# Performance work log

Measured on AMD Instinct MI355X. Metric: run time of the kernel, lower is better.

Reference implementation:

```python
import jax, jax.numpy as jnp
import numpy as np

D_MODEL = 1024
NUM_EXPERTS = 64
TOP_K = 2
TEMPERATURE = 1.0


def setup_inputs() -> dict:
    key = jax.random.key(0)
    k1, k2, k3, k4 = jax.random.split(key, 4)
    mh_output = jax.random.normal(k1, (8, 4096, D_MODEL), dtype=jnp.float32)
    noise = jax.random.normal(k2, (8, 4096, NUM_EXPERTS), dtype=jnp.float32)  # randn_like sample, externalized
    # nn.Linear weights: shape [out, in], init normal(0, 0.02); biases zero
    W_route = jax.random.normal(k3, (NUM_EXPERTS, D_MODEL), dtype=jnp.float32) * 0.02
    b_route = jnp.zeros((NUM_EXPERTS,), dtype=jnp.float32)
    W_noise = jax.random.normal(k4, (NUM_EXPERTS, D_MODEL), dtype=jnp.float32) * 0.02
    b_noise = jnp.zeros((NUM_EXPERTS,), dtype=jnp.float32)
    return {"mh_output": mh_output, "noise": noise, "W_route": W_route,
            "b_route": b_route, "W_noise": W_noise, "b_noise": b_noise}


def reference(mh_output, noise, W_route, b_route, W_noise, b_noise):
    # logits = topkroute_linear(mh_output); noise_logits = noise_linear(mh_output)
    logits = jnp.einsum('bsd,ed->bse', mh_output, W_route) + b_route
    noise_logits = jnp.einsum('bsd,ed->bse', mh_output, W_noise) + b_noise
    # noisy logits = logits + temperature * randn * softplus(noise_logits)
    noisy = logits + TEMPERATURE * noise * jax.nn.softplus(noise_logits)
    # top-k, scatter into -inf, softmax  ==  softmax over top-k values scattered into zeros
    top_vals, indices = jax.lax.top_k(noisy, TOP_K)          # [b, s, k]
    probs_k = jax.nn.softmax(top_vals, axis=-1)              # softmax(-inf elsewhere) -> 0 elsewhere
    one_hot = jax.nn.one_hot(indices, NUM_EXPERTS, dtype=noisy.dtype)  # [b, s, k, E]
    router_output = jnp.sum(one_hot * probs_k[..., None], axis=-2)     # [b, s, E]
    return router_output, indices
```

## Files before the change

### kernel.cpp

```cpp
#include <hip/hip_runtime.h>
#include <math.h>


#define T_TOKENS 32768
#define D_MODEL  1024
#define NE       64
#define NCOL     128
#define M_TILE   32
#define NCHUNK   (D_MODEL / 32)
#define CS_LD    68
#define OUT_IDX_BASE ((size_t)T_TOKENS * NE)
#define W_ELEMS  (NCOL * D_MODEL)

typedef short  bf16x8  __attribute__((ext_vector_type(8)));
typedef float  floatx4 __attribute__((ext_vector_type(4)));

__device__ __forceinline__ unsigned short f32_to_bf16_rne(float x) {
    unsigned u = __float_as_uint(x);
    unsigned r = u + 0x7fffu + ((u >> 16) & 1u);
    return (unsigned short)(r >> 16);
}
__device__ __forceinline__ float bf16_bits_to_f32(unsigned short h) {
    return __uint_as_float(((unsigned)h) << 16);
}
__device__ __forceinline__ int4 pack8(const unsigned short* h) {
    int4 r;
    r.x = (int)((unsigned)h[0] | ((unsigned)h[1] << 16));
    r.y = (int)((unsigned)h[2] | ((unsigned)h[3] << 16));
    r.z = (int)((unsigned)h[4] | ((unsigned)h[5] << 16));
    r.w = (int)((unsigned)h[6] | ((unsigned)h[7] << 16));
    return r;
}
__device__ __forceinline__ float softplus_f(float x) {
    return fmaxf(x, 0.f) + log1pf(expf(-fabsf(x)));
}

__global__ __launch_bounds__(256) void prepack_w(
    const float* __restrict__ Wr, const float* __restrict__ Wn,
    short* __restrict__ Bh, short* __restrict__ Bl)
{
    int g   = blockIdx.x * 256 + threadIdx.x;
    int n   = g & 15;
    int kg  = (g >> 4) & 127;
    int t2  = g >> 11;
    int col = t2 * 16 + n;
    const float* src = (col < NE ? Wr + (size_t)col * D_MODEL
                                 : Wn + (size_t)(col - NE) * D_MODEL) + kg * 8;
    float4 a = *(const float4*)src;
    float4 b = *(const float4*)(src + 4);
    float v[8] = {a.x, a.y, a.z, a.w, b.x, b.y, b.z, b.w};
    unsigned short h[8], l[8];
    #pragma unroll
    for (int j = 0; j < 8; ++j) {
        h[j] = f32_to_bf16_rne(v[j]);
        l[j] = f32_to_bf16_rne(v[j] - bf16_bits_to_f32(h[j]));
    }
    *(int4*)(Bh + (size_t)g * 8) = pack8(h);
    *(int4*)(Bl + (size_t)g * 8) = pack8(l);
}

__global__ __launch_bounds__(256, 4) void router_mfma(
    const float* __restrict__ A,
    const float* __restrict__ noise,
    const float* __restrict__ br,
    const float* __restrict__ bn,
    const short* __restrict__ Bh,
    const short* __restrict__ Bl,
    float* __restrict__ out)
{
    __shared__ float Cs[M_TILE * CS_LD];
    __shared__ float s_p1[M_TILE], s_p2[M_TILE];
    __shared__ int   s_e1[M_TILE], s_e2[M_TILE];

    const int tid  = threadIdx.x;
    const int lane = tid & 63;
    const int wid  = tid >> 6;
    const int wm   = wid & 1;
    const int wn   = wid >> 1;
    const int n16  = lane & 15;
    const int quad = lane >> 4;
    const int m0   = blockIdx.x * M_TILE;

    const float* pA = A + (size_t)(m0 + wm * 16 + n16) * D_MODEL + quad * 8;

    int bBase[4];
    #pragma unroll
    for (int f = 0; f < 4; ++f) {
        int ntile = (f < 2) ? (wn * 2 + f) : (4 + wn * 2 + (f - 2));
        bBase[f] = ((ntile * 128 + quad) * 16 + n16) * 8;
    }

    floatx4 acc[4];
    #pragma unroll
    for (int f = 0; f < 4; ++f) acc[f] = (floatx4)0.f;

    float4 aC0 = *(const float4*)(pA);
    float4 aC1 = *(const float4*)(pA + 4);
    float4 aN0 = *(const float4*)(pA + 32);
    float4 aN1 = *(const float4*)(pA + 36);

    for (int kc = 0; kc < NCHUNK; ++kc) {
        float4 aF0, aF1;
        if (kc + 2 < NCHUNK) {
            aF0 = *(const float4*)(pA + (kc + 2) * 32);
            aF1 = *(const float4*)(pA + (kc + 2) * 32 + 4);
        }
        bf16x8 bh[4], bl[4];
        #pragma unroll
        for (int f = 0; f < 4; ++f) {
            size_t o = (size_t)bBase[f] + (size_t)kc * 512;
            bh[f] = *(const bf16x8*)(Bh + o);
            bl[f] = *(const bf16x8*)(Bl + o);
        }
        float v[8] = {aC0.x, aC0.y, aC0.z, aC0.w, aC1.x, aC1.y, aC1.z, aC1.w};
        bf16x8 afh, afl;
        #pragma unroll
        for (int j = 0; j < 8; ++j) {
            unsigned short h = f32_to_bf16_rne(v[j]);
            afh[j] = (short)h;
            afl[j] = (short)f32_to_bf16_rne(v[j] - bf16_bits_to_f32(h));
        }
        #pragma unroll
        for (int f = 0; f < 4; ++f) {
            acc[f] = __builtin_amdgcn_mfma_f32_16x16x32_bf16(afh, bh[f], acc[f], 0, 0, 0);
            acc[f] = __builtin_amdgcn_mfma_f32_16x16x32_bf16(afh, bl[f], acc[f], 0, 0, 0);
            acc[f] = __builtin_amdgcn_mfma_f32_16x16x32_bf16(afl, bh[f], acc[f], 0, 0, 0);
        }
        aC0 = aN0; aC1 = aN1; aN0 = aF0; aN1 = aF1;
    }

    #pragma unroll
    for (int nfi = 0; nfi < 2; ++nfi) {
        int e = wn * 32 + nfi * 16 + n16;
        float brv = br[e], bnv = bn[e];
        #pragma unroll
        for (int r = 0; r < 4; ++r) {
            int t = wm * 16 + quad * 4 + r;
            float nz    = noise[(size_t)(m0 + t) * NE + e];
            float route = acc[nfi][r]     + brv;
            float nl    = acc[2 + nfi][r] + bnv;
            Cs[t * CS_LD + e] = fmaf(nz, softplus_f(nl), route);
        }
    }
    __syncthreads();

    if (tid < M_TILE) {
        const int t = tid;
        float v1 = -INFINITY, v2 = -INFINITY;
        int e1 = 0, e2 = 0;
        #pragma unroll 8
        for (int e = 0; e < NE; ++e) {
            float v = Cs[t * CS_LD + e];
            if (v > v1) { v2 = v1; e2 = e1; v1 = v; e1 = e; }
            else if (v > v2) { v2 = v; e2 = e; }
        }
        float ex = expf(v2 - v1);
        float denom = 1.f + ex;
        s_p1[t] = 1.f / denom;
        s_p2[t] = ex / denom;
        s_e1[t] = e1;
        s_e2[t] = e2;
        float2 iv = make_float2((float)e1, (float)e2);
        *(float2*)(out + OUT_IDX_BASE + (size_t)(m0 + t) * 2) = iv;
    }
    __syncthreads();

    #pragma unroll
    for (int i = 0; i < 2; ++i) {
        int gi = i * 256 + tid;
        int t  = gi >> 4;
        int e0 = (gi & 15) * 4;
        float p1 = s_p1[t], p2 = s_p2[t];
        int   e1 = s_e1[t], e2 = s_e2[t];
        float4 v;
        v.x = (e0 + 0 == e1) ? p1 : ((e0 + 0 == e2) ? p2 : 0.f);
        v.y = (e0 + 1 == e1) ? p1 : ((e0 + 1 == e2) ? p2 : 0.f);
        v.z = (e0 + 2 == e1) ? p1 : ((e0 + 2 == e2) ? p2 : 0.f);
        v.w = (e0 + 3 == e1) ? p1 : ((e0 + 3 == e2) ? p2 : 0.f);
        *(float4*)(out + (size_t)(m0 + t) * NE + e0) = v;
    }
}

extern "C" void kernel_launch(void* const* d_in, const int* in_sizes, int n_in,
                              void* d_out, int out_size, void* d_ws, size_t ws_size,
                              hipStream_t stream) {
    const float* A     = (const float*)d_in[0];
    const float* noise = (const float*)d_in[1];
    const float* Wr    = (const float*)d_in[2];
    const float* br    = (const float*)d_in[3];
    const float* Wn    = (const float*)d_in[4];
    const float* bn    = (const float*)d_in[5];
    float* out = (float*)d_out;

    short* Bh = (short*)d_ws;
    short* Bl = Bh + W_ELEMS;

    prepack_w<<<dim3(W_ELEMS / 8 / 256), dim3(256), 0, stream>>>(Wr, Wn, Bh, Bl);
    router_mfma<<<dim3(T_TOKENS / M_TILE), dim3(256), 0, stream>>>(A, noise, br, bn, Bh, Bl, out);
}
```

Baseline: 268.9 us.

## Stage A tile as split bf16 in double-buffered LDS shared by all waves

Each thread now loads one float4 of the activation tile, converts it to hi/lo bf16 once, and writes it to a double-buffered shared-memory tile. Waves read the A fragments from there. Previously every wave converted its own A fragments, so the same conversion was repeated across waves. The wave split changes from 2x2 (M x N) to 4 waves over N, so each wave covers both 16-row M fragments with a single route/noise column tile, and the B fragments are prefetched one chunk ahead. The cost is a block barrier every K chunk and extra LDS traffic.

New measurement: 232.6 us. 1.16x faster.

```diff
diff --git a/kernel.cpp b/kernel.cpp
--- a/kernel.cpp
+++ b/kernel.cpp
@@ -22,14 +22,6 @@
 }
 __device__ __forceinline__ float bf16_bits_to_f32(unsigned short h) {
     return __uint_as_float(((unsigned)h) << 16);
-}
-__device__ __forceinline__ int4 pack8(const unsigned short* h) {
-    int4 r;
-    r.x = (int)((unsigned)h[0] | ((unsigned)h[1] << 16));
-    r.y = (int)((unsigned)h[2] | ((unsigned)h[3] << 16));
-    r.z = (int)((unsigned)h[4] | ((unsigned)h[5] << 16));
-    r.w = (int)((unsigned)h[6] | ((unsigned)h[7] << 16));
-    return r;
 }
 __device__ __forceinline__ float softplus_f(float x) {
     return fmaxf(x, 0.f) + log1pf(expf(-fabsf(x)));
@@ -55,8 +47,17 @@
         h[j] = f32_to_bf16_rne(v[j]);
         l[j] = f32_to_bf16_rne(v[j] - bf16_bits_to_f32(h[j]));
     }
-    *(int4*)(Bh + (size_t)g * 8) = pack8(h);
-    *(int4*)(Bl + (size_t)g * 8) = pack8(l);
+    int4 hp, lp;
+    hp.x = (int)((unsigned)h[0] | ((unsigned)h[1] << 16));
+    hp.y = (int)((unsigned)h[2] | ((unsigned)h[3] << 16));
+    hp.z = (int)((unsigned)h[4] | ((unsigned)h[5] << 16));
+    hp.w = (int)((unsigned)h[6] | ((unsigned)h[7] << 16));
+    lp.x = (int)((unsigned)l[0] | ((unsigned)l[1] << 16));
+    lp.y = (int)((unsigned)l[2] | ((unsigned)l[3] << 16));
+    lp.z = (int)((unsigned)l[4] | ((unsigned)l[5] << 16));
+    lp.w = (int)((unsigned)l[6] | ((unsigned)l[7] << 16));
+    *(int4*)(Bh + (size_t)g * 8) = hp;
+    *(int4*)(Bl + (size_t)g * 8) = lp;
 }
 
 __global__ __launch_bounds__(256, 4) void router_mfma(
@@ -68,6 +69,8 @@
     const short* __restrict__ Bl,
     float* __restrict__ out)
 {
+    __shared__ __align__(16) short Ah[2][M_TILE * 32];
+    __shared__ __align__(16) short Al[2][M_TILE * 32];
     __shared__ float Cs[M_TILE * CS_LD];
     __shared__ float s_p1[M_TILE], s_p2[M_TILE];
     __shared__ int   s_e1[M_TILE], s_e2[M_TILE];
@@ -75,72 +78,107 @@
     const int tid  = threadIdx.x;
     const int lane = tid & 63;
     const int wid  = tid >> 6;
-    const int wm   = wid & 1;
-    const int wn   = wid >> 1;
     const int n16  = lane & 15;
     const int quad = lane >> 4;
     const int m0   = blockIdx.x * M_TILE;
 
-    const float* pA = A + (size_t)(m0 + wm * 16 + n16) * D_MODEL + quad * 8;
-
-    int bBase[4];
+    const int ms = tid >> 3;
+    const int kq = tid & 7;
+    const float* pA = A + (size_t)(m0 + ms) * D_MODEL + kq * 4;
+    const int sBase = ((kq >> 1) * M_TILE + ms) * 8 + (kq & 1) * 4;
+
+    const int bBaseR = ((wid * 128 + quad) * 16 + n16) * 8;
+    const int bBaseN = (((4 + wid) * 128 + quad) * 16 + n16) * 8;
+
+    floatx4 acc[2][2];
     #pragma unroll
-    for (int f = 0; f < 4; ++f) {
-        int ntile = (f < 2) ? (wn * 2 + f) : (4 + wn * 2 + (f - 2));
-        bBase[f] = ((ntile * 128 + quad) * 16 + n16) * 8;
-    }
-
-    floatx4 acc[4];
-    #pragma unroll
-    for (int f = 0; f < 4; ++f) acc[f] = (floatx4)0.f;
-
-    float4 aC0 = *(const float4*)(pA);
-    float4 aC1 = *(const float4*)(pA + 4);
-    float4 aN0 = *(const float4*)(pA + 32);
-    float4 aN1 = *(const float4*)(pA + 36);
+    for (int i = 0; i < 2; ++i) { acc[i][0] = (floatx4)0.f; acc[i][1] = (floatx4)0.f; }
+
+#define CONVERT_STORE(buf_, f4_) do {                                       \
+        float v_[4] = {(f4_).x, (f4_).y, (f4_).z, (f4_).w};                  \
+        unsigned short h_[4], l_[4];                                         \
+        _Pragma("unroll")                                                    \
+        for (int j_ = 0; j_ < 4; ++j_) {                                     \
+            h_[j_] = f32_to_bf16_rne(v_[j_]);                                \
+            l_[j_] = f32_to_bf16_rne(v_[j_] - bf16_bits_to_f32(h_[j_]));     \
+        }                                                                    \
+        int2 hp_, lp_;                                                       \
+        hp_.x = (int)((unsigned)h_[0] | ((unsigned)h_[1] << 16));            \
+        hp_.y = (int)((unsigned)h_[2] | ((unsigned)h_[3] << 16));            \
+        lp_.x = (int)((unsigned)l_[0] | ((unsigned)l_[1] << 16));            \
+        lp_.y = (int)((unsigned)l_[2] | ((unsigned)l_[3] << 16));            \
+        *(int2*)&Ah[(buf_)][sBase] = hp_;                                    \
+        *(int2*)&Al[(buf_)][sBase] = lp_;                                    \
+    } while (0)
+
+    {
+        float4 a0 = *(const float4*)pA;
+        CONVERT_STORE(0, a0);
+    }
+    bf16x8 bhR, blR, bhN, blN;
+    bhR = *(const bf16x8*)(Bh + bBaseR);
+    blR = *(const bf16x8*)(Bl + bBaseR);
+    bhN = *(const bf16x8*)(Bh + bBaseN);
+    blN = *(const bf16x8*)(Bl + bBaseN);
+    float4 aP1 = *(const float4*)(pA + 32);
+    __syncthreads();
 
     for (int kc = 0; kc < NCHUNK; ++kc) {
-        float4 aF0, aF1;
-        if (kc + 2 < NCHUNK) {
-            aF0 = *(const float4*)(pA + (kc + 2) * 32);
-            aF1 = *(const float4*)(pA + (kc + 2) * 32 + 4);
-        }
-        bf16x8 bh[4], bl[4];
+        const int cur = kc & 1, nxt = cur ^ 1;
+
+        float4 aP2;
+        if (kc + 2 < NCHUNK)
+            aP2 = *(const float4*)(pA + (kc + 2) * 32);
+
+        bf16x8 bhRn, blRn, bhNn, blNn;
+        if (kc + 1 < NCHUNK) {
+            int o = (kc + 1) * 512;
+            bhRn = *(const bf16x8*)(Bh + bBaseR + o);
+            blRn = *(const bf16x8*)(Bl + bBaseR + o);
+            bhNn = *(const bf16x8*)(Bh + bBaseN + o);
+            blNn = *(const bf16x8*)(Bl + bBaseN + o);
+        }
+
+        bf16x8 afh[2], afl[2];
         #pragma unroll
-        for (int f = 0; f < 4; ++f) {
-            size_t o = (size_t)bBase[f] + (size_t)kc * 512;
-            bh[f] = *(const bf16x8*)(Bh + o);
-            bl[f] = *(const bf16x8*)(Bl + o);
-        }
-        float v[8] = {aC0.x, aC0.y, aC0.z, aC0.w, aC1.x, aC1.y, aC1.z, aC1.w};
-        bf16x8 afh, afl;
+        for (int mf = 0; mf < 2; ++mf) {
+            int g = (quad * M_TILE + mf * 16 + n16) * 8;
+            afh[mf] = *(const bf16x8*)&Ah[cur][g];
+            afl[mf] = *(const bf16x8*)&Al[cur][g];
+        }
+
         #pragma unroll
-        for (int j = 0; j < 8; ++j) {
-            unsigned short h = f32_to_bf16_rne(v[j]);
-            afh[j] = (short)h;
-            afl[j] = (short)f32_to_bf16_rne(v[j] - bf16_bits_to_f32(h));
-        }
-        #pragma unroll
-        for (int f = 0; f < 4; ++f) {
-            acc[f] = __builtin_amdgcn_mfma_f32_16x16x32_bf16(afh, bh[f], acc[f], 0, 0, 0);
-            acc[f] = __builtin_amdgcn_mfma_f32_16x16x32_bf16(afh, bl[f], acc[f], 0, 0, 0);
-            acc[f] = __builtin_amdgcn_mfma_f32_16x16x32_bf16(afl, bh[f], acc[f], 0, 0, 0);
-        }
-        aC0 = aN0; aC1 = aN1; aN0 = aF0; aN1 = aF1;
-    }
-
-    #pragma unroll
-    for (int nfi = 0; nfi < 2; ++nfi) {
-        int e = wn * 32 + nfi * 16 + n16;
+        for (int mf = 0; mf < 2; ++mf) {
+            acc[mf][0] = __builtin_amdgcn_mfma_f32_16x16x32_bf16(afh[mf], bhR, acc[mf][0], 0, 0, 0);
+            acc[mf][0] = __builtin_amdgcn_mfma_f32_16x16x32_bf16(afh[mf], blR, acc[mf][0], 0, 0, 0);
+            acc[mf][0] = __builtin_amdgcn_mfma_f32_16x16x32_bf16(afl[mf], bhR, acc[mf][0], 0, 0, 0);
+            acc[mf][1] = __builtin_amdgcn_mfma_f32_16x16x32_bf16(afh[mf], bhN, acc[mf][1], 0, 0, 0);
+            acc[mf][1] = __builtin_amdgcn_mfma_f32_16x16x32_bf16(afh[mf], blN, acc[mf][1], 0, 0, 0);
+            acc[mf][1] = __builtin_amdgcn_mfma_f32_16x16x32_bf16(afl[mf], bhN, acc[mf][1], 0, 0, 0);
+        }
+
+        if (kc + 1 < NCHUNK)
+            CONVERT_STORE(nxt, aP1);
+
+        __syncthreads();
+
+        aP1 = aP2;
+        bhR = bhRn; blR = blRn; bhN = bhNn; blN = blNn;
+    }
+
+    {
+        int e = wid * 16 + n16;
         float brv = br[e], bnv = bn[e];
         #pragma unroll
-        for (int r = 0; r < 4; ++r) {
-            int t = wm * 16 + quad * 4 + r;
-            float nz    = noise[(size_t)(m0 + t) * NE + e];
-            float route = acc[nfi][r]     + brv;
-            float nl    = acc[2 + nfi][r] + bnv;
-            Cs[t * CS_LD + e] = fmaf(nz, softplus_f(nl), route);
-        }
+        for (int mf = 0; mf < 2; ++mf)
+            #pragma unroll
+            for (int r = 0; r < 4; ++r) {
+                int t = mf * 16 + quad * 4 + r;
+                float nz    = noise[(size_t)(m0 + t) * NE + e];
+                float route = acc[mf][0][r] + brv;
+                float nl    = acc[mf][1][r] + bnv;
+                Cs[t * CS_LD + e] = fmaf(nz, softplus_f(nl), route);
+            }
     }
     __syncthreads();
 
```
